# Kernel optimization log

Hardware: AMD Instinct MI355X
Metric: run time of the kernel (lower is better)

Reference implementation:

```python
import jax, jax.numpy as jnp
import numpy as np

N_P, N_A = 200_000, 100_000
D_P, D_A, H, OUT = 64, 64, 32, 1
E_PP, E_AP, E_PA = 3_200_000, 1_600_000, 1_600_000


def _lin(key, din, dout, bias=True):
    kw, kb = jax.random.split(key)
    W = jax.random.normal(kw, (din, dout), jnp.float32) * (1.0 / np.sqrt(din))
    if bias:
        b = jax.random.normal(kb, (dout,), jnp.float32) * 0.01
        return W, b
    return W


def setup_inputs() -> dict:
    key = jax.random.key(0)
    ks = jax.random.split(key, 24)
    inp = {}
    inp['x_paper'] = jax.random.normal(ks[0], (N_P, D_P), jnp.float32)
    inp['x_author'] = jax.random.normal(ks[1], (N_A, D_A), jnp.float32)
    inp['src_pp'] = jax.random.randint(ks[2], (E_PP,), 0, N_P)
    inp['dst_pp'] = jax.random.randint(ks[3], (E_PP,), 0, N_P)
    inp['src_ap'] = jax.random.randint(ks[4], (E_AP,), 0, N_A)
    inp['dst_ap'] = jax.random.randint(ks[5], (E_AP,), 0, N_P)
    inp['src_pa'] = jax.random.randint(ks[6], (E_PA,), 0, N_P)
    inp['dst_pa'] = jax.random.randint(ks[7], (E_PA,), 0, N_A)
    # Layer-1 SAGEConv weights per relation: lin_l (neighbor, with bias), lin_r (root, no bias)
    inp['Wl1_pp'], inp['bl1_pp'] = _lin(ks[8], D_P, H)
    inp['Wr1_pp'] = _lin(ks[9], D_P, H, bias=False)
    inp['Wl1_ap'], inp['bl1_ap'] = _lin(ks[10], D_A, H)
    inp['Wr1_ap'] = _lin(ks[11], D_P, H, bias=False)
    inp['Wl1_pa'], inp['bl1_pa'] = _lin(ks[12], D_P, H)
    inp['Wr1_pa'] = _lin(ks[13], D_A, H, bias=False)
    # Layer-2 SAGEConv weights (only relations feeding 'paper' affect the output)
    inp['Wl2_pp'], inp['bl2_pp'] = _lin(ks[14], H, H)
    inp['Wr2_pp'] = _lin(ks[15], H, H, bias=False)
    inp['Wl2_ap'], inp['bl2_ap'] = _lin(ks[16], H, H)
    inp['Wr2_ap'] = _lin(ks[17], H, H, bias=False)
    # Final classifier Linear(32, 1)
    inp['W_lin'], inp['b_lin'] = _lin(ks[18], H, OUT)
    return inp


def _sage_rel(x_src, x_dst, src, dst, Wl, bl, Wr):
    # SAGEConv: lin_l(mean_{j in N(i)} x_j) + lin_r(x_i)
    n_dst = x_dst.shape[0]
    agg = jax.ops.segment_sum(x_src[src], dst, num_segments=n_dst)
    cnt = jax.ops.segment_sum(jnp.ones((src.shape[0],), x_src.dtype), dst, num_segments=n_dst)
    mean = agg / jnp.maximum(cnt, 1.0)[:, None]
    return mean @ Wl + bl + x_dst @ Wr


def reference(x_paper, x_author, src_pp, dst_pp, src_ap, dst_ap, src_pa, dst_pa,
              Wl1_pp, bl1_pp, Wr1_pp, Wl1_ap, bl1_ap, Wr1_ap, Wl1_pa, bl1_pa, Wr1_pa,
              Wl2_pp, bl2_pp, Wr2_pp, Wl2_ap, bl2_ap, Wr2_ap, W_lin, b_lin):
    # Layer 1 (to_hetero: sum per-relation conv outputs per destination type), then relu
    p1 = (_sage_rel(x_paper, x_paper, src_pp, dst_pp, Wl1_pp, bl1_pp, Wr1_pp)
          + _sage_rel(x_author, x_paper, src_ap, dst_ap, Wl1_ap, bl1_ap, Wr1_ap))
    a1 = _sage_rel(x_paper, x_author, src_pa, dst_pa, Wl1_pa, bl1_pa, Wr1_pa)
    p1, a1 = jax.nn.relu(p1), jax.nn.relu(a1)
    # Layer 2: only 'paper' output is consumed downstream
    p2 = (_sage_rel(p1, p1, src_pp, dst_pp, Wl2_pp, bl2_pp, Wr2_pp)
          + _sage_rel(a1, p1, src_ap, dst_ap, Wl2_ap, bl2_ap, Wr2_ap))
    # model_config is None -> plain Linear, no sigmoid/softmax
    return p2 @ W_lin + b_lin
```

## Files before the change

kernel.cpp:

```cpp
#include <hip/hip_runtime.h>


typedef unsigned short ushort_t;
typedef __attribute__((ext_vector_type(8))) short bf16x8;
typedef __attribute__((ext_vector_type(4))) float f32x4;

#define PWBITS 9
#define PWIN   (1 << PWBITS)
#define PCHUNK 4096
#define CAPPAD 2048
#define FW_R   12

__device__ inline ushort_t f2bf(float f) {
    unsigned u = __float_as_uint(f);
    unsigned r = (u + 0x7FFFu + ((u >> 16) & 1u)) >> 16;
    return (ushort_t)r;
}
__device__ inline float bf2f_lo(unsigned u) { return __uint_as_float(u << 16); }
__device__ inline float bf2f_hi(unsigned u) { return __uint_as_float(u & 0xFFFF0000u); }
__device__ inline int ntl(const int* p) { return __builtin_nontemporal_load(p); }

__global__ void prep_weights(
    const float* __restrict__ Wl1_pp, const float* __restrict__ Wr1_pp,
    const float* __restrict__ Wl1_ap, const float* __restrict__ Wr1_ap,
    const float* __restrict__ Wl1_pa, const float* __restrict__ Wr1_pa,
    const float* __restrict__ bl1_pp, const float* __restrict__ bl1_ap,
    const float* __restrict__ bl1_pa,
    const float* __restrict__ Wl2_pp, const float* __restrict__ bl2_pp,
    const float* __restrict__ Wr2_pp,
    const float* __restrict__ Wl2_ap, const float* __restrict__ bl2_ap,
    const float* __restrict__ Wr2_ap,
    const float* __restrict__ W_lin, const float* __restrict__ b_lin,
    float* __restrict__ Wcomb_p, float* __restrict__ Wcomb_a,
    ushort_t* __restrict__ Wfrag_p, ushort_t* __restrict__ Wfrag_a,
    float* __restrict__ bias_p, float* __restrict__ bias_a,
    float* __restrict__ vv)
{
    int t = threadIdx.x;
    for (int idx = t; idx < 64 * 96; idx += 256) {
        int i = idx / 96, j = idx % 96;
        float v;
        if (j < 32)       v = Wl1_pp[i * 32 + j];
        else if (j < 64)  v = Wl1_pa[i * 32 + (j - 32)];
        else              v = Wr1_pp[i * 32 + (j - 64)] + Wr1_ap[i * 32 + (j - 64)];
        Wcomb_p[idx] = v;
    }
    for (int idx = t; idx < 64 * 64; idx += 256) {
        int i = idx / 64, j = idx % 64;
        Wcomb_a[idx] = (j < 32) ? Wl1_ap[i * 32 + j] : Wr1_pa[i * 32 + (j - 32)];
    }
    if (t < 32) {
        bias_p[t] = bl1_pp[t] + bl1_ap[t];
        bias_a[t] = bl1_pa[t];
        float vpp = 0.f, vr = 0.f, vap = 0.f;
        for (int j = 0; j < 32; ++j) {
            float wl = W_lin[j];
            vpp += Wl2_pp[t * 32 + j] * wl;
            vr  += (Wr2_pp[t * 32 + j] + Wr2_ap[t * 32 + j]) * wl;
            vap += Wl2_ap[t * 32 + j] * wl;
        }
        vv[t] = vpp; vv[32 + t] = vr; vv[96 + t] = vap;
    }
    if (t == 0) {
        float c = b_lin[0];
        for (int j = 0; j < 32; ++j) c += (bl2_pp[j] + bl2_ap[j]) * W_lin[j];
        vv[64] = c;
    }
    __syncthreads();
    for (int idx = t; idx < 12 * 64 * 8; idx += 256) {
        int f = idx >> 9, l = (idx >> 3) & 63, j = idx & 7;
        int nt = f >> 1, kh = f & 1;
        int k = kh * 32 + 8 * (l >> 4) + j;
        int n = nt * 16 + (l & 15);
        Wfrag_p[idx] = f2bf(Wcomb_p[k * 96 + n]);
    }
    for (int idx = t; idx < 8 * 64 * 8; idx += 256) {
        int f = idx >> 9, l = (idx >> 3) & 63, j = idx & 7;
        int nt = f >> 1, kh = f & 1;
        int k = kh * 32 + 8 * (l >> 4) + j;
        int n = nt * 16 + (l & 15);
        Wfrag_a[idx] = f2bf(Wcomb_a[k * 64 + n]);
    }
}

__device__ inline void partition_body(
    int b, int nb0, int nb1,
    const int* __restrict__ src0, const int* __restrict__ dst0, int E0,
    unsigned* __restrict__ bk0, int cap0, int nw0, int* __restrict__ wc0,
    const int* __restrict__ src1, const int* __restrict__ dst1, int E1,
    unsigned* __restrict__ bk1, int cap1, int nw1, int* __restrict__ wc1,
    const int* __restrict__ src2, const int* __restrict__ dst2, int E2,
    unsigned* __restrict__ bk2, int cap2, int nw2, int* __restrict__ wc2,
    int* lcnt, int* lbase)
{
    const int* src; const int* dst; int E; unsigned* bk; int cap; int nw; int* wc; int chunk;
    if (b < nb0)            { src = src0; dst = dst0; E = E0; bk = bk0; cap = cap0; nw = nw0; wc = wc0; chunk = b; }
    else if (b < nb0 + nb1) { src = src1; dst = dst1; E = E1; bk = bk1; cap = cap1; nw = nw1; wc = wc1; chunk = b - nb0; }
    else                    { src = src2; dst = dst2; E = E2; bk = bk2; cap = cap2; nw = nw2; wc = wc2; chunk = b - nb0 - nb1; }
    int e0 = chunk * PCHUNK;
    int d_[16], s_[16];
#pragma unroll
    for (int r = 0; r < 4; ++r) {
        int base = e0 + r * 1024 + threadIdx.x * 4;
        if (base + 3 < E) {
            int4 dv = *(const int4*)(dst + base);
            int4 sv = *(const int4*)(src + base);
            d_[r * 4 + 0] = dv.x; d_[r * 4 + 1] = dv.y; d_[r * 4 + 2] = dv.z; d_[r * 4 + 3] = dv.w;
            s_[r * 4 + 0] = sv.x; s_[r * 4 + 1] = sv.y; s_[r * 4 + 2] = sv.z; s_[r * 4 + 3] = sv.w;
        } else {
#pragma unroll
            for (int k = 0; k < 4; ++k) {
                int e = base + k;
                d_[r * 4 + k] = (e < E) ? dst[e] : -1;
                s_[r * 4 + k] = 0;
            }
        }
    }
    for (int i = threadIdx.x; i < nw; i += 256) lcnt[i] = 0;
    __syncthreads();
#pragma unroll
    for (int k = 0; k < 16; ++k)
        if (d_[k] >= 0) atomicAdd(&lcnt[((unsigned)d_[k]) >> PWBITS], 1);
    __syncthreads();
    for (int i = threadIdx.x; i < nw; i += 256) {
        int c = lcnt[i];
        lbase[i] = (c > 0) ? atomicAdd(&wc[i * 16], c) : 0;
        lcnt[i] = 0;
    }
    __syncthreads();
#pragma unroll
    for (int k = 0; k < 16; ++k) {
        int d = d_[k];
        if (d >= 0) {
            int w = ((unsigned)d) >> PWBITS;
            int off = lbase[w] + atomicAdd(&lcnt[w], 1);
            if (off < cap)
                bk[(size_t)w * cap + off] =
                    (((unsigned)(d & (PWIN - 1))) << 18) | (unsigned)s_[k];
        }
    }
}

__device__ inline bf16x8 cvt8(const float* p) {
    float4 a = *(const float4*)p;
    float4 b = *(const float4*)(p + 4);
    bf16x8 r;
    r[0] = (short)f2bf(a.x); r[1] = (short)f2bf(a.y);
    r[2] = (short)f2bf(a.z); r[3] = (short)f2bf(a.w);
    r[4] = (short)f2bf(b.x); r[5] = (short)f2bf(b.y);
    r[6] = (short)f2bf(b.z); r[7] = (short)f2bf(b.w);
    return r;
}

__device__ inline void proj_paper_body(
    int blk, const float* __restrict__ x, const ushort_t* __restrict__ Wfrag,
    const float* __restrict__ bias,
    ushort_t* __restrict__ h_pp, ushort_t* __restrict__ h_pa,
    float* __restrict__ root_p, int N)
{
    int wave = threadIdx.x >> 6, lane = threadIdx.x & 63;
    int mbase = blk * 64 + wave * 16;
    int row = lane & 15, grp = lane >> 4;
    int nA = mbase + row; if (nA > N - 1) nA = N - 1;
    const float* xr = x + (size_t)nA * 64 + grp * 8;
    bf16x8 a0 = cvt8(xr);
    bf16x8 a1 = cvt8(xr + 32);
    f32x4 acc0 = {0.f, 0.f, 0.f, 0.f}, acc1 = acc0, acc2 = acc0, acc3 = acc0;
    float bp0 = bias[row];
    float bp1 = bias[16 + row];
    f32x4 acc4 = {bp0, bp0, bp0, bp0};
    f32x4 acc5 = {bp1, bp1, bp1, bp1};
    const bf16x8* wf = (const bf16x8*)(Wfrag) + lane;
    acc0 = __builtin_amdgcn_mfma_f32_16x16x32_bf16(a0, wf[0 * 64], acc0, 0, 0, 0);
    acc0 = __builtin_amdgcn_mfma_f32_16x16x32_bf16(a1, wf[1 * 64], acc0, 0, 0, 0);
    acc1 = __builtin_amdgcn_mfma_f32_16x16x32_bf16(a0, wf[2 * 64], acc1, 0, 0, 0);
    acc1 = __builtin_amdgcn_mfma_f32_16x16x32_bf16(a1, wf[3 * 64], acc1, 0, 0, 0);
    acc2 = __builtin_amdgcn_mfma_f32_16x16x32_bf16(a0, wf[4 * 64], acc2, 0, 0, 0);
    acc2 = __builtin_amdgcn_mfma_f32_16x16x32_bf16(a1, wf[5 * 64], acc2, 0, 0, 0);
    acc3 = __builtin_amdgcn_mfma_f32_16x16x32_bf16(a0, wf[6 * 64], acc3, 0, 0, 0);
    acc3 = __builtin_amdgcn_mfma_f32_16x16x32_bf16(a1, wf[7 * 64], acc3, 0, 0, 0);
    acc4 = __builtin_amdgcn_mfma_f32_16x16x32_bf16(a0, wf[8 * 64], acc4, 0, 0, 0);
    acc4 = __builtin_amdgcn_mfma_f32_16x16x32_bf16(a1, wf[9 * 64], acc4, 0, 0, 0);
    acc5 = __builtin_amdgcn_mfma_f32_16x16x32_bf16(a0, wf[10 * 64], acc5, 0, 0, 0);
    acc5 = __builtin_amdgcn_mfma_f32_16x16x32_bf16(a1, wf[11 * 64], acc5, 0, 0, 0);
    int node0 = mbase + grp * 4;
#pragma unroll
    for (int reg = 0; reg < 4; ++reg) {
        int nd = node0 + reg;
        if (nd < N) {
            size_t b32 = (size_t)nd * 32;
            h_pp[b32 + row]        = f2bf(acc0[reg]);
            h_pp[b32 + 16 + row]   = f2bf(acc1[reg]);
            h_pa[b32 + row]        = f2bf(acc2[reg]);
            h_pa[b32 + 16 + row]   = f2bf(acc3[reg]);
            root_p[b32 + row]      = acc4[reg];
            root_p[b32 + 16 + row] = acc5[reg];
        }
    }
}

__device__ inline void proj_author_body(
    int blk, const float* __restrict__ x, const ushort_t* __restrict__ Wfrag,
    const float* __restrict__ bias,
    ushort_t* __restrict__ h_ap, float* __restrict__ root_a, int N)
{
    int wave = threadIdx.x >> 6, lane = threadIdx.x & 63;
    int mbase = blk * 64 + wave * 16;
    int row = lane & 15, grp = lane >> 4;
    int nA = mbase + row; if (nA > N - 1) nA = N - 1;
    const float* xr = x + (size_t)nA * 64 + grp * 8;
    bf16x8 a0 = cvt8(xr);
    bf16x8 a1 = cvt8(xr + 32);
    f32x4 acc0 = {0.f, 0.f, 0.f, 0.f}, acc1 = acc0;
    float bp0 = bias[row];
    float bp1 = bias[16 + row];
    f32x4 acc2 = {bp0, bp0, bp0, bp0};
    f32x4 acc3 = {bp1, bp1, bp1, bp1};
    const bf16x8* wf = (const bf16x8*)(Wfrag) + lane;
    acc0 = __builtin_amdgcn_mfma_f32_16x16x32_bf16(a0, wf[0 * 64], acc0, 0, 0, 0);
    acc0 = __builtin_amdgcn_mfma_f32_16x16x32_bf16(a1, wf[1 * 64], acc0, 0, 0, 0);
    acc1 = __builtin_amdgcn_mfma_f32_16x16x32_bf16(a0, wf[2 * 64], acc1, 0, 0, 0);
    acc1 = __builtin_amdgcn_mfma_f32_16x16x32_bf16(a1, wf[3 * 64], acc1, 0, 0, 0);
    acc2 = __builtin_amdgcn_mfma_f32_16x16x32_bf16(a0, wf[4 * 64], acc2, 0, 0, 0);
    acc2 = __builtin_amdgcn_mfma_f32_16x16x32_bf16(a1, wf[5 * 64], acc2, 0, 0, 0);
    acc3 = __builtin_amdgcn_mfma_f32_16x16x32_bf16(a0, wf[6 * 64], acc3, 0, 0, 0);
    acc3 = __builtin_amdgcn_mfma_f32_16x16x32_bf16(a1, wf[7 * 64], acc3, 0, 0, 0);
    int node0 = mbase + grp * 4;
#pragma unroll
    for (int reg = 0; reg < 4; ++reg) {
        int nd = node0 + reg;
        if (nd < N) {
            size_t b32 = (size_t)nd * 32;
            h_ap[b32 + row]        = f2bf(acc0[reg]);
            h_ap[b32 + 16 + row]   = f2bf(acc1[reg]);
            root_a[b32 + row]      = acc2[reg];
            root_a[b32 + 16 + row] = acc3[reg];
        }
    }
}

__global__ __launch_bounds__(256)
void part_proj(
    const int* __restrict__ src0, const int* __restrict__ dst0, int E0,
    unsigned* __restrict__ bk0, int cap0, int nw0, int* __restrict__ wc0,
    const int* __restrict__ src1, const int* __restrict__ dst1, int E1,
    unsigned* __restrict__ bk1, int cap1, int nw1, int* __restrict__ wc1,
    const int* __restrict__ src2, const int* __restrict__ dst2, int E2,
    unsigned* __restrict__ bk2, int cap2, int nw2, int* __restrict__ wc2,
    const float* __restrict__ xp, const float* __restrict__ xa,
    const ushort_t* __restrict__ Wfp, const ushort_t* __restrict__ Wfa,
    const float* __restrict__ bias_p, const float* __restrict__ bias_a,
    ushort_t* __restrict__ h_pp, ushort_t* __restrict__ h_pa,
    ushort_t* __restrict__ h_ap,
    float* __restrict__ root_p, float* __restrict__ root_a,
    int NP, int NA, int nbt, int pbp)
{
    __shared__ int lcnt[PWIN];
    __shared__ int lbase[PWIN];
    int b = blockIdx.x;
    int nb0 = (E0 + PCHUNK - 1) / PCHUNK;
    int nb1 = (E1 + PCHUNK - 1) / PCHUNK;
    if (b < nbt) {
        partition_body(b, nb0, nb1,
                       src0, dst0, E0, bk0, cap0, nw0, wc0,
                       src1, dst1, E1, bk1, cap1, nw1, wc1,
                       src2, dst2, E2, bk2, cap2, nw2, wc2, lcnt, lbase);
    } else if (b < nbt + pbp) {
        proj_paper_body(b - nbt, xp, Wfp, bias_p, h_pp, h_pa, root_p, NP);
    } else {
        proj_author_body(b - nbt - pbp, xa, Wfa, bias_a, h_ap, root_a, NA);
    }
}

__global__ __launch_bounds__(256)
void partition3(
    const int* __restrict__ src0, const int* __restrict__ dst0, int E0,
    unsigned* __restrict__ bk0, int cap0, int nw0, int* __restrict__ wc0,
    const int* __restrict__ src1, const int* __restrict__ dst1, int E1,
    unsigned* __restrict__ bk1, int cap1, int nw1, int* __restrict__ wc1,
    const int* __restrict__ src2, const int* __restrict__ dst2, int E2,
    unsigned* __restrict__ bk2, int cap2, int nw2, int* __restrict__ wc2)
{
    __shared__ int lcnt[PWIN];
    __shared__ int lbase[PWIN];
    int nb0 = (E0 + PCHUNK - 1) / PCHUNK;
    int nb1 = (E1 + PCHUNK - 1) / PCHUNK;
    partition_body(blockIdx.x, nb0, nb1,
                   src0, dst0, E0, bk0, cap0, nw0, wc0,
                   src1, dst1, E1, bk1, cap1, nw1, wc1,
                   src2, dst2, E2, bk2, cap2, nw2, wc2, lcnt, lbase);
}

__global__ __launch_bounds__(256)
void proj_all(const float* __restrict__ xp, const float* __restrict__ xa,
              const ushort_t* __restrict__ Wfp, const ushort_t* __restrict__ Wfa,
              const float* __restrict__ bias_p, const float* __restrict__ bias_a,
              ushort_t* __restrict__ h_pp, ushort_t* __restrict__ h_pa,
              ushort_t* __restrict__ h_ap,
              float* __restrict__ root_p, float* __restrict__ root_a,
              int NP, int NA, int pbp)
{
    if (blockIdx.x < pbp)
        proj_paper_body(blockIdx.x, xp, Wfp, bias_p, h_pp, h_pa, root_p, NP);
    else
        proj_author_body(blockIdx.x - pbp, xa, Wfa, bias_a, h_ap, root_a, NA);
}

__global__ __launch_bounds__(256)
void fill_win3(
    const unsigned* __restrict__ bk0, const int* __restrict__ wc0, int cap0,
    int* __restrict__ csr0, int* __restrict__ cnt0, int* __restrict__ rs0, int N0, int nw0,
    const unsigned* __restrict__ bk1, const int* __restrict__ wc1, int cap1,
    int* __restrict__ csr1, int* __restrict__ cnt1, int* __restrict__ rs1, int N1, int nw1,
    const unsigned* __restrict__ bk2, const int* __restrict__ wc2, int cap2,
    int* __restrict__ csr2, int* __restrict__ cnt2, int* __restrict__ rs2, int N2, int nw2)
{
    __shared__ int lc[PWIN];
    __shared__ int wsum[4], wpre[4];
    int b = blockIdx.x;
    const unsigned* bk; const int* wc; int cap; int* csr; int* cnt; int* rs; int N; int w;
    if (b < nw0)            { bk = bk0; wc = wc0; cap = cap0; csr = csr0; cnt = cnt0; rs = rs0; N = N0; w = b; }
    else if (b < nw0 + nw1) { bk = bk1; wc = wc1; cap = cap1; csr = csr1; cnt = cnt1; rs = rs1; N = N1; w = b - nw0; }
    else                    { bk = bk2; wc = wc2; cap = cap2; csr = csr2; cnt = cnt2; rs = rs2; N = N2; w = b - nw0 - nw1; }
    int d0 = w << PWBITS;
    int sz = wc[w * 16]; if (sz > cap) sz = cap;
    const unsigned* bkt = bk + (size_t)w * cap;
    uint4 u[FW_R];
#pragma unroll
    for (int r = 0; r < FW_R; ++r) {
        int i4 = r * 1024 + threadIdx.x * 4;
        if (i4 + 3 < sz) {
            u[r] = *(const uint4*)(bkt + i4);
        } else {
            u[r].x = (i4 + 0 < sz) ? bkt[i4 + 0] : 0xFFFFFFFFu;
            u[r].y = (i4 + 1 < sz) ? bkt[i4 + 1] : 0xFFFFFFFFu;
            u[r].z = (i4 + 2 < sz) ? bkt[i4 + 2] : 0xFFFFFFFFu;
            u[r].w = (i4 + 3 < sz) ? bkt[i4 + 3] : 0xFFFFFFFFu;
        }
    }
    for (int i = threadIdx.x; i < PWIN; i += 256) lc[i] = 0;
    __syncthreads();
#pragma unroll
    for (int r = 0; r < FW_R; ++r) {
        if (u[r].x != 0xFFFFFFFFu) atomicAdd(&lc[u[r].x >> 18], 1);
        if (u[r].y != 0xFFFFFFFFu) atomicAdd(&lc[u[r].y >> 18], 1);
        if (u[r].z != 0xFFFFFFFFu) atomicAdd(&lc[u[r].z >> 18], 1);
        if (u[r].w != 0xFFFFFFFFu) atomicAdd(&lc[u[r].w >> 18], 1);
    }
    __syncthreads();
    {
        int i = threadIdx.x * 2;
        int d = d0 + i;
        if (d < N)     cnt[d] = lc[i];
        if (d + 1 < N) cnt[d + 1] = lc[i + 1];
    }
    int t2 = threadIdx.x * 2;
    int v0 = lc[t2], v1 = lc[t2 + 1];
    int ts = v0 + v1;
    int lane = threadIdx.x & 63;
    int wid = threadIdx.x >> 6;
    int incl = ts;
#pragma unroll
    for (int off = 1; off < 64; off <<= 1) {
        int o = __shfl_up(incl, off);
        if (lane >= off) incl += o;
    }
    if (lane == 63) wsum[wid] = incl;
    __syncthreads();
    if (threadIdx.x == 0) {
        int r = 0;
        for (int i = 0; i < 4; ++i) { wpre[i] = r; r += wsum[i]; }
    }
    __syncthreads();
    int run = w * cap + wpre[wid] + (incl - ts);
    lc[t2] = run;
    if (d0 + t2 < N) rs[d0 + t2] = run;
    run += v0;
    lc[t2 + 1] = run;
    if (d0 + t2 + 1 < N) rs[d0 + t2 + 1] = run;
    __syncthreads();
#pragma unroll
    for (int r = 0; r < FW_R; ++r) {
        if (u[r].x != 0xFFFFFFFFu) { int p = atomicAdd(&lc[u[r].x >> 18], 1); csr[p] = (int)(u[r].x & 0x3FFFFu); }
        if (u[r].y != 0xFFFFFFFFu) { int p = atomicAdd(&lc[u[r].y >> 18], 1); csr[p] = (int)(u[r].y & 0x3FFFFu); }
        if (u[r].z != 0xFFFFFFFFu) { int p = atomicAdd(&lc[u[r].z >> 18], 1); csr[p] = (int)(u[r].z & 0x3FFFFu); }
        if (u[r].w != 0xFFFFFFFFu) { int p = atomicAdd(&lc[u[r].w >> 18], 1); csr[p] = (int)(u[r].w & 0x3FFFFu); }
    }
}

#define ACC8(A, U) \
    A[0] += bf2f_lo((U).x); A[1] += bf2f_hi((U).x); \
    A[2] += bf2f_lo((U).y); A[3] += bf2f_hi((U).y); \
    A[4] += bf2f_lo((U).z); A[5] += bf2f_hi((U).z); \
    A[6] += bf2f_lo((U).w); A[7] += bf2f_hi((U).w);

__global__ __launch_bounds__(256, 8)
void pull_paper(const ushort_t* __restrict__ h_pp, const ushort_t* __restrict__ h_ap,
                const float* __restrict__ root,
                const int* __restrict__ csr_pp, const int* __restrict__ rs_pp,
                const int* __restrict__ cnt_pp,
                const int* __restrict__ csr_ap, const int* __restrict__ rs_ap,
                const int* __restrict__ cnt_ap,
                const float* __restrict__ vv,
                float* __restrict__ s_pp, float* __restrict__ out, int N)
{
    __shared__ float v0[32], v1[32];
    __shared__ float c2s;
    if (threadIdx.x < 32) { v0[threadIdx.x] = vv[threadIdx.x]; v1[threadIdx.x] = vv[32 + threadIdx.x]; }
    if (threadIdx.x == 0) c2s = vv[64];
    __syncthreads();
    int n = blockIdx.x * 64 + (threadIdx.x >> 2);
    if (n >= N) return;
    int c = threadIdx.x & 3;
    float a[8];
#pragma unroll
    for (int k = 0; k < 8; ++k) a[k] = 0.f;
    int s1 = rs_pp[n], k1 = cnt_pp[n], e1 = s1 + k1;
    int j = s1;
    for (; j + 4 <= e1; j += 4) {
        int i0 = ntl(csr_pp + j), i1 = ntl(csr_pp + j + 1);
        int i2 = ntl(csr_pp + j + 2), i3 = ntl(csr_pp + j + 3);
        uint4 u0 = ((const uint4*)(h_pp + (size_t)i0 * 32))[c];
        uint4 u1 = ((const uint4*)(h_pp + (size_t)i1 * 32))[c];
        uint4 u2 = ((const uint4*)(h_pp + (size_t)i2 * 32))[c];
        uint4 u3 = ((const uint4*)(h_pp + (size_t)i3 * 32))[c];
        ACC8(a, u0) ACC8(a, u1) ACC8(a, u2) ACC8(a, u3)
    }
    for (; j < e1; ++j) {
        uint4 u0 = ((const uint4*)(h_pp + (size_t)ntl(csr_pp + j) * 32))[c];
        ACC8(a, u0)
    }
    float b[8];
#pragma unroll
    for (int k = 0; k < 8; ++k) b[k] = 0.f;
    int s2 = rs_ap[n], k2 = cnt_ap[n], e2 = s2 + k2;
    j = s2;
    for (; j + 4 <= e2; j += 4) {
        int i0 = ntl(csr_ap + j), i1 = ntl(csr_ap + j + 1);
        int i2 = ntl(csr_ap + j + 2), i3 = ntl(csr_ap + j + 3);
        uint4 u0 = ((const uint4*)(h_ap + (size_t)i0 * 32))[c];
        uint4 u1 = ((const uint4*)(h_ap + (size_t)i1 * 32))[c];
        uint4 u2 = ((const uint4*)(h_ap + (size_t)i2 * 32))[c];
        uint4 u3 = ((const uint4*)(h_ap + (size_t)i3 * 32))[c];
        ACC8(b, u0) ACC8(b, u1) ACC8(b, u2) ACC8(b, u3)
    }
    for (; j < e2; ++j) {
        uint4 u0 = ((const uint4*)(h_ap + (size_t)ntl(csr_ap + j) * 32))[c];
        ACC8(b, u0)
    }
    float ipp = 1.0f / fmaxf((float)k1, 1.0f);
    float iap = 1.0f / fmaxf((float)k2, 1.0f);
    const float* rt = root + (size_t)n * 32 + 8 * c;
    float d0 = 0.f, d1 = 0.f;
#pragma unroll
    for (int k = 0; k < 8; ++k) {
        float p = fmaxf(rt[k] + a[k] * ipp + b[k] * iap, 0.f);
        d0 += p * v0[8 * c + k];
        d1 += p * v1[8 * c + k];
    }
    d0 += __shfl_xor(d0, 1); d0 += __shfl_xor(d0, 2);
    d1 += __shfl_xor(d1, 1); d1 += __shfl_xor(d1, 2);
    if (c == 0) { s_pp[n] = d0; out[n] = d1 + c2s; }
}

__global__ __launch_bounds__(256, 8)
void pull_author(const ushort_t* __restrict__ h_pa, const float* __restrict__ root,
                 const int* __restrict__ csr_pa, const int* __restrict__ rs_pa,
                 const int* __restrict__ cnt_pa,
                 const float* __restrict__ vv, float* __restrict__ s_ap, int N)
{
    __shared__ float v0[32];
    if (threadIdx.x < 32) v0[threadIdx.x] = vv[96 + threadIdx.x];
    __syncthreads();
    int n = blockIdx.x * 64 + (threadIdx.x >> 2);
    if (n >= N) return;
    int c = threadIdx.x & 3;
    float a[8];
#pragma unroll
    for (int k = 0; k < 8; ++k) a[k] = 0.f;
    int s1 = rs_pa[n], k1 = cnt_pa[n], e1 = s1 + k1;
    int j = s1;
    for (; j + 4 <= e1; j += 4) {
        int i0 = ntl(csr_pa + j), i1 = ntl(csr_pa + j + 1);
        int i2 = ntl(csr_pa + j + 2), i3 = ntl(csr_pa + j + 3);
        uint4 u0 = ((const uint4*)(h_pa + (size_t)i0 * 32))[c];
        uint4 u1 = ((const uint4*)(h_pa + (size_t)i1 * 32))[c];
        uint4 u2 = ((const uint4*)(h_pa + (size_t)i2 * 32))[c];
        uint4 u3 = ((const uint4*)(h_pa + (size_t)i3 * 32))[c];
        ACC8(a, u0) ACC8(a, u1) ACC8(a, u2) ACC8(a, u3)
    }
    for (; j < e1; ++j) {
        uint4 u0 = ((const uint4*)(h_pa + (size_t)ntl(csr_pa + j) * 32))[c];
        ACC8(a, u0)
    }
    float ip = 1.0f / fmaxf((float)k1, 1.0f);
    const float* rt = root + (size_t)n * 32 + 8 * c;
    float d0 = 0.f;
#pragma unroll
    for (int k = 0; k < 8; ++k) {
        float p = fmaxf(rt[k] + a[k] * ip, 0.f);
        d0 += p * v0[8 * c + k];
    }
    d0 += __shfl_xor(d0, 1); d0 += __shfl_xor(d0, 2);
    if (c == 0) s_ap[n] = d0;
}

__global__ __launch_bounds__(256, 8)
void pull2(const float* __restrict__ s_pp, const float* __restrict__ s_ap,
           const int* __restrict__ csr_pp, const int* __restrict__ rs_pp,
           const int* __restrict__ cnt_pp,
           const int* __restrict__ csr_ap, const int* __restrict__ rs_ap,
           const int* __restrict__ cnt_ap,
           float* __restrict__ out, int N)
{
    int g = (blockIdx.x * blockDim.x + threadIdx.x) >> 2;
    int c = threadIdx.x & 3;
    if (g >= N) return;
    int s1 = rs_pp[g], k1 = cnt_pp[g], e1 = s1 + k1;
    float t = 0.f;
    for (int j = s1 + c; j < e1; j += 4) t += s_pp[ntl(csr_pp + j)];
    int s2 = rs_ap[g], k2 = cnt_ap[g], e2 = s2 + k2;
    float u = 0.f;
    for (int j = s2 + c; j < e2; j += 4) u += s_ap[ntl(csr_ap + j)];
    t += __shfl_xor(t, 1); t += __shfl_xor(t, 2);
    u += __shfl_xor(u, 1); u += __shfl_xor(u, 2);
    if (c == 0) {
        out[g] += t / fmaxf((float)k1, 1.f) + u / fmaxf((float)k2, 1.f);
    }
}

extern "C" void kernel_launch(void* const* d_in, const int* in_sizes, int n_in,
                              void* d_out, int out_size, void* d_ws, size_t ws_size,
                              hipStream_t stream)
{
    const float* x_paper  = (const float*)d_in[0];
    const float* x_author = (const float*)d_in[1];
    const int* src_pp = (const int*)d_in[2];
    const int* dst_pp = (const int*)d_in[3];
    const int* src_ap = (const int*)d_in[4];
    const int* dst_ap = (const int*)d_in[5];
    const int* src_pa = (const int*)d_in[6];
    const int* dst_pa = (const int*)d_in[7];
    const float* Wl1_pp = (const float*)d_in[8];
    const float* bl1_pp = (const float*)d_in[9];
    const float* Wr1_pp = (const float*)d_in[10];
    const float* Wl1_ap = (const float*)d_in[11];
    const float* bl1_ap = (const float*)d_in[12];
    const float* Wr1_ap = (const float*)d_in[13];
    const float* Wl1_pa = (const float*)d_in[14];
    const float* bl1_pa = (const float*)d_in[15];
    const float* Wr1_pa = (const float*)d_in[16];
    const float* Wl2_pp = (const float*)d_in[17];
    const float* bl2_pp = (const float*)d_in[18];
    const float* Wr2_pp = (const float*)d_in[19];
    const float* Wl2_ap = (const float*)d_in[20];
    const float* bl2_ap = (const float*)d_in[21];
    const float* Wr2_ap = (const float*)d_in[22];
    const float* W_lin  = (const float*)d_in[23];
    const float* b_lin  = (const float*)d_in[24];

    const int NP = in_sizes[0] / 64;
    const int NA = in_sizes[1] / 64;
    const int E_PP = in_sizes[2];
    const int E_AP = in_sizes[4];
    const int E_PA = in_sizes[6];

    const int nw_pp = (NP + PWIN - 1) >> PWBITS;
    const int nw_ap = nw_pp;
    const int nw_pa = (NA + PWIN - 1) >> PWBITS;
    const int cap_pp = ((E_PP / nw_pp + CAPPAD) + 3) & ~3;
    const int cap_ap = ((E_AP / nw_ap + CAPPAD) + 3) & ~3;
    const int cap_pa = ((E_PA / nw_pa + CAPPAD) + 3) & ~3;

    char* wp = (char*)d_ws;
    int* wcur = (int*)wp;             wp += (size_t)3 * PWIN * 16 * 4;
    unsigned* bk_pp = (unsigned*)wp;  wp += (size_t)nw_pp * cap_pp * 4;
    unsigned* bk_ap = (unsigned*)wp;  wp += (size_t)nw_ap * cap_ap * 4;
    unsigned* bk_pa = (unsigned*)wp;  wp += (size_t)nw_pa * cap_pa * 4;
    int* csr_pp = (int*)wp;           wp += (size_t)nw_pp * cap_pp * 4;
    int* csr_ap = (int*)wp;           wp += (size_t)nw_ap * cap_ap * 4;
    int* csr_pa = (int*)wp;           wp += (size_t)nw_pa * cap_pa * 4;
    int* cnt    = (int*)wp;           wp += (size_t)(2 * NP + NA) * 4;
    int* rs     = (int*)wp;           wp += (size_t)(2 * NP + NA) * 4;
    ushort_t* h_pp = (ushort_t*)wp;   wp += (size_t)NP * 32 * 2;
    ushort_t* h_pa = (ushort_t*)wp;   wp += (size_t)NP * 32 * 2;
    ushort_t* h_ap = (ushort_t*)wp;   wp += (size_t)NA * 32 * 2;
    float* root_a = (float*)wp;       wp += (size_t)NA * 32 * 4;
    float* s_pp   = (float*)wp;       wp += (size_t)NP * 4;
    float* s_ap   = (float*)wp;       wp += (size_t)NA * 4;
    float* Wcomb_p = (float*)wp;      wp += 64 * 96 * 4;
    float* Wcomb_a = (float*)wp;      wp += 64 * 64 * 4;
    ushort_t* Wfrag_p = (ushort_t*)wp; wp += 12 * 64 * 8 * 2;
    ushort_t* Wfrag_a = (ushort_t*)wp; wp += 8 * 64 * 8 * 2;
    float* bias_p = (float*)wp;       wp += 32 * 4;
    float* bias_a = (float*)wp;       wp += 32 * 4;
    float* vv     = (float*)wp;       wp += 128 * 4;
    size_t used = (size_t)(wp - (char*)d_ws);
    size_t rootp_bytes = (size_t)NP * 32 * 4;
    bool fused = (used + rootp_bytes) <= ws_size;
    float* root_p = fused ? (float*)wp : (float*)bk_pp;

    int* cnt_pp = cnt,  * cnt_ap = cnt + NP,  * cnt_pa = cnt + 2 * NP;
    int* rs_pp  = rs,   * rs_ap  = rs + NP,   * rs_pa  = rs + 2 * NP;

    float* out = (float*)d_out;

    hipMemsetAsync(wcur, 0, (size_t)3 * PWIN * 16 * 4, stream);

    prep_weights<<<1, 256, 0, stream>>>(
        Wl1_pp, Wr1_pp, Wl1_ap, Wr1_ap, Wl1_pa, Wr1_pa,
        bl1_pp, bl1_ap, bl1_pa,
        Wl2_pp, bl2_pp, Wr2_pp, Wl2_ap, bl2_ap, Wr2_ap,
        W_lin, b_lin, Wcomb_p, Wcomb_a, Wfrag_p, Wfrag_a, bias_p, bias_a, vv);

    int nb_total = (E_PP + PCHUNK - 1) / PCHUNK + (E_AP + PCHUNK - 1) / PCHUNK
                 + (E_PA + PCHUNK - 1) / PCHUNK;
    int pbp = (NP + 63) / 64;
    int pba = (NA + 63) / 64;

    if (fused) {
        part_proj<<<nb_total + pbp + pba, 256, 0, stream>>>(
            src_pp, dst_pp, E_PP, bk_pp, cap_pp, nw_pp, wcur + 0,
            src_ap, dst_ap, E_AP, bk_ap, cap_ap, nw_ap, wcur + PWIN * 16,
            src_pa, dst_pa, E_PA, bk_pa, cap_pa, nw_pa, wcur + 2 * PWIN * 16,
            x_paper, x_author, Wfrag_p, Wfrag_a, bias_p, bias_a,
            h_pp, h_pa, h_ap, root_p, root_a, NP, NA, nb_total, pbp);

        fill_win3<<<nw_pp + nw_ap + nw_pa, 256, 0, stream>>>(
            bk_pp, wcur + 0,             cap_pp, csr_pp, cnt_pp, rs_pp, NP, nw_pp,
            bk_ap, wcur + PWIN * 16,     cap_ap, csr_ap, cnt_ap, rs_ap, NP, nw_ap,
            bk_pa, wcur + 2 * PWIN * 16, cap_pa, csr_pa, cnt_pa, rs_pa, NA, nw_pa);
    } else {
        partition3<<<nb_total, 256, 0, stream>>>(
            src_pp, dst_pp, E_PP, bk_pp, cap_pp, nw_pp, wcur + 0,
            src_ap, dst_ap, E_AP, bk_ap, cap_ap, nw_ap, wcur + PWIN * 16,
            src_pa, dst_pa, E_PA, bk_pa, cap_pa, nw_pa, wcur + 2 * PWIN * 16);

        fill_win3<<<nw_pp + nw_ap + nw_pa, 256, 0, stream>>>(
            bk_pp, wcur + 0,             cap_pp, csr_pp, cnt_pp, rs_pp, NP, nw_pp,
            bk_ap, wcur + PWIN * 16,     cap_ap, csr_ap, cnt_ap, rs_ap, NP, nw_ap,
            bk_pa, wcur + 2 * PWIN * 16, cap_pa, csr_pa, cnt_pa, rs_pa, NA, nw_pa);

        proj_all<<<pbp + pba, 256, 0, stream>>>(
            x_paper, x_author, Wfrag_p, Wfrag_a, bias_p, bias_a,
            h_pp, h_pa, h_ap, root_p, root_a, NP, NA, pbp);
    }

    pull_paper<<<(NP + 63) / 64, 256, 0, stream>>>(
        h_pp, h_ap, root_p, csr_pp, rs_pp, cnt_pp, csr_ap, rs_ap, cnt_ap,
        vv, s_pp, out, NP);
    pull_author<<<(NA + 63) / 64, 256, 0, stream>>>(
        h_pa, root_a, csr_pa, rs_pa, cnt_pa, vv, s_ap, NA);

    pull2<<<((size_t)NP * 4 + 255) / 256, 256, 0, stream>>>(
        s_pp, s_ap, csr_pp, rs_pp, cnt_pp, csr_ap, rs_ap, cnt_ap, out, NP);
}
```

Before: 367.6 us.

## Fuse projection blocks with CSR fill instead of with edge partition

Before, the node projection GEMM blocks ran in the same launch as the edge partition pass, and the CSR window fill ran in a separate launch afterward. Now partition runs alone, and the projection blocks share a launch with the window-fill blocks. This pairs the atomic-heavy, LDS-bound fill blocks with MFMA/bandwidth projection blocks, and leaves partition with full occupancy. The fallback path reuses the fused kernel with block counts chosen so only one role runs per launch. The risk is that fill is shorter or less parallel than partition (a few hundred blocks), which would hide less of the projection work than before.

```diff
diff --git a/kernel.cpp b/kernel.cpp
--- a/kernel.cpp
+++ b/kernel.cpp
@@ -83,16 +83,20 @@
     }
 }
 
-__device__ inline void partition_body(
-    int b, int nb0, int nb1,
+__global__ __launch_bounds__(256)
+void partition3(
     const int* __restrict__ src0, const int* __restrict__ dst0, int E0,
     unsigned* __restrict__ bk0, int cap0, int nw0, int* __restrict__ wc0,
     const int* __restrict__ src1, const int* __restrict__ dst1, int E1,
     unsigned* __restrict__ bk1, int cap1, int nw1, int* __restrict__ wc1,
     const int* __restrict__ src2, const int* __restrict__ dst2, int E2,
-    unsigned* __restrict__ bk2, int cap2, int nw2, int* __restrict__ wc2,
-    int* lcnt, int* lbase)
-{
+    unsigned* __restrict__ bk2, int cap2, int nw2, int* __restrict__ wc2)
+{
+    __shared__ int lcnt[PWIN];
+    __shared__ int lbase[PWIN];
+    int nb0 = (E0 + PCHUNK - 1) / PCHUNK;
+    int nb1 = (E1 + PCHUNK - 1) / PCHUNK;
+    int b = blockIdx.x;
     const int* src; const int* dst; int E; unsigned* bk; int cap; int nw; int* wc; int chunk;
     if (b < nb0)            { src = src0; dst = dst0; E = E0; bk = bk0; cap = cap0; nw = nw0; wc = wc0; chunk = b; }
     else if (b < nb0 + nb1) { src = src1; dst = dst1; E = E1; bk = bk1; cap = cap1; nw = nw1; wc = wc1; chunk = b - nb0; }
@@ -138,6 +142,77 @@
                 bk[(size_t)w * cap + off] =
                     (((unsigned)(d & (PWIN - 1))) << 18) | (unsigned)s_[k];
         }
+    }
+}
+
+__device__ inline void fill_body(
+    int b, const unsigned* __restrict__ bk, const int* __restrict__ wc, int cap,
+    int* __restrict__ csr, int* __restrict__ cnt, int* __restrict__ rs,
+    int N, int w, int* lc, int* wsum, int* wpre)
+{
+    int d0 = w << PWBITS;
+    int sz = wc[w * 16]; if (sz > cap) sz = cap;
+    const unsigned* bkt = bk + (size_t)w * cap;
+    uint4 u[FW_R];
+#pragma unroll
+    for (int r = 0; r < FW_R; ++r) {
+        int i4 = r * 1024 + threadIdx.x * 4;
+        if (i4 + 3 < sz) {
+            u[r] = *(const uint4*)(bkt + i4);
+        } else {
+            u[r].x = (i4 + 0 < sz) ? bkt[i4 + 0] : 0xFFFFFFFFu;
+            u[r].y = (i4 + 1 < sz) ? bkt[i4 + 1] : 0xFFFFFFFFu;
+            u[r].z = (i4 + 2 < sz) ? bkt[i4 + 2] : 0xFFFFFFFFu;
+            u[r].w = (i4 + 3 < sz) ? bkt[i4 + 3] : 0xFFFFFFFFu;
+        }
+    }
+    for (int i = threadIdx.x; i < PWIN; i += 256) lc[i] = 0;
+    __syncthreads();
+#pragma unroll
+    for (int r = 0; r < FW_R; ++r) {
+        if (u[r].x != 0xFFFFFFFFu) atomicAdd(&lc[u[r].x >> 18], 1);
+        if (u[r].y != 0xFFFFFFFFu) atomicAdd(&lc[u[r].y >> 18], 1);
+        if (u[r].z != 0xFFFFFFFFu) atomicAdd(&lc[u[r].z >> 18], 1);
+        if (u[r].w != 0xFFFFFFFFu) atomicAdd(&lc[u[r].w >> 18], 1);
+    }
+    __syncthreads();
+    {
+        int i = threadIdx.x * 2;
+        int d = d0 + i;
+        if (d < N)     cnt[d] = lc[i];
+        if (d + 1 < N) cnt[d + 1] = lc[i + 1];
+    }
+    int t2 = threadIdx.x * 2;
+    int v0 = lc[t2], v1 = lc[t2 + 1];
+    int ts = v0 + v1;
+    int lane = threadIdx.x & 63;
+    int wid = threadIdx.x >> 6;
+    int incl = ts;
+#pragma unroll
+    for (int off = 1; off < 64; off <<= 1) {
+        int o = __shfl_up(incl, off);
+        if (lane >= off) incl += o;
+    }
+    if (lane == 63) wsum[wid] = incl;
+    __syncthreads();
+    if (threadIdx.x == 0) {
+        int r = 0;
+        for (int i = 0; i < 4; ++i) { wpre[i] = r; r += wsum[i]; }
+    }
+    __syncthreads();
+    int run = w * cap + wpre[wid] + (incl - ts);
+    lc[t2] = run;
+    if (d0 + t2 < N) rs[d0 + t2] = run;
+    run += v0;
+    lc[t2 + 1] = run;
+    if (d0 + t2 + 1 < N) rs[d0 + t2 + 1] = run;
+    __syncthreads();
+#pragma unroll
+    for (int r = 0; r < FW_R; ++r) {
+        if (u[r].x != 0xFFFFFFFFu) { int p = atomicAdd(&lc[u[r].x >> 18], 1); csr[p] = (int)(u[r].x & 0x3FFFFu); }
+        if (u[r].y != 0xFFFFFFFFu) { int p = atomicAdd(&lc[u[r].y >> 18], 1); csr[p] = (int)(u[r].y & 0x3FFFFu); }
+        if (u[r].z != 0xFFFFFFFFu) { int p = atomicAdd(&lc[u[r].z >> 18], 1); csr[p] = (int)(u[r].z & 0x3FFFFu); }
+        if (u[r].w != 0xFFFFFFFFu) { int p = atomicAdd(&lc[u[r].w >> 18], 1); csr[p] = (int)(u[r].w & 0x3FFFFu); }
     }
 }
 
@@ -240,151 +315,35 @@
 }
 
 __global__ __launch_bounds__(256)
-void part_proj(
-    const int* __restrict__ src0, const int* __restrict__ dst0, int E0,
-    unsigned* __restrict__ bk0, int cap0, int nw0, int* __restrict__ wc0,
-    const int* __restrict__ src1, const int* __restrict__ dst1, int E1,
-    unsigned* __restrict__ bk1, int cap1, int nw1, int* __restrict__ wc1,
-    const int* __restrict__ src2, const int* __restrict__ dst2, int E2,
-    unsigned* __restrict__ bk2, int cap2, int nw2, int* __restrict__ wc2,
+void fill_proj(
+    const unsigned* __restrict__ bk0, const int* __restrict__ wc0, int cap0,
+    int* __restrict__ csr0, int* __restrict__ cnt0, int* __restrict__ rs0, int N0, int nw0,
+    const unsigned* __restrict__ bk1, const int* __restrict__ wc1, int cap1,
+    int* __restrict__ csr1, int* __restrict__ cnt1, int* __restrict__ rs1, int N1, int nw1,
+    const unsigned* __restrict__ bk2, const int* __restrict__ wc2, int cap2,
+    int* __restrict__ csr2, int* __restrict__ cnt2, int* __restrict__ rs2, int N2, int nw2,
     const float* __restrict__ xp, const float* __restrict__ xa,
     const ushort_t* __restrict__ Wfp, const ushort_t* __restrict__ Wfa,
     const float* __restrict__ bias_p, const float* __restrict__ bias_a,
     ushort_t* __restrict__ h_pp, ushort_t* __restrict__ h_pa,
     ushort_t* __restrict__ h_ap,
     float* __restrict__ root_p, float* __restrict__ root_a,
-    int NP, int NA, int nbt, int pbp)
-{
-    __shared__ int lcnt[PWIN];
-    __shared__ int lbase[PWIN];
-    int b = blockIdx.x;
-    int nb0 = (E0 + PCHUNK - 1) / PCHUNK;
-    int nb1 = (E1 + PCHUNK - 1) / PCHUNK;
-    if (b < nbt) {
-        partition_body(b, nb0, nb1,
-                       src0, dst0, E0, bk0, cap0, nw0, wc0,
-                       src1, dst1, E1, bk1, cap1, nw1, wc1,
-                       src2, dst2, E2, bk2, cap2, nw2, wc2, lcnt, lbase);
-    } else if (b < nbt + pbp) {
-        proj_paper_body(b - nbt, xp, Wfp, bias_p, h_pp, h_pa, root_p, NP);
-    } else {
-        proj_author_body(b - nbt - pbp, xa, Wfa, bias_a, h_ap, root_a, NA);
-    }
-}
-
-__global__ __launch_bounds__(256)
-void partition3(
-    const int* __restrict__ src0, const int* __restrict__ dst0, int E0,
-    unsigned* __restrict__ bk0, int cap0, int nw0, int* __restrict__ wc0,
-    const int* __restrict__ src1, const int* __restrict__ dst1, int E1,
-    unsigned* __restrict__ bk1, int cap1, int nw1, int* __restrict__ wc1,
-    const int* __restrict__ src2, const int* __restrict__ dst2, int E2,
-    unsigned* __restrict__ bk2, int cap2, int nw2, int* __restrict__ wc2)
-{
-    __shared__ int lcnt[PWIN];
-    __shared__ int lbase[PWIN];
-    int nb0 = (E0 + PCHUNK - 1) / PCHUNK;
-    int nb1 = (E1 + PCHUNK - 1) / PCHUNK;
-    partition_body(blockIdx.x, nb0, nb1,
-                   src0, dst0, E0, bk0, cap0, nw0, wc0,
-                   src1, dst1, E1, bk1, cap1, nw1, wc1,
-                   src2, dst2, E2, bk2, cap2, nw2, wc2, lcnt, lbase);
-}
-
-__global__ __launch_bounds__(256)
-void proj_all(const float* __restrict__ xp, const float* __restrict__ xa,
-              const ushort_t* __restrict__ Wfp, const ushort_t* __restrict__ Wfa,
-              const float* __restrict__ bias_p, const float* __restrict__ bias_a,
-              ushort_t* __restrict__ h_pp, ushort_t* __restrict__ h_pa,
-              ushort_t* __restrict__ h_ap,
-              float* __restrict__ root_p, float* __restrict__ root_a,
-              int NP, int NA, int pbp)
-{
-    if (blockIdx.x < pbp)
-        proj_paper_body(blockIdx.x, xp, Wfp, bias_p, h_pp, h_pa, root_p, NP);
-    else
-        proj_author_body(blockIdx.x - pbp, xa, Wfa, bias_a, h_ap, root_a, NA);
-}
-
-__global__ __launch_bounds__(256)
-void fill_win3(
-    const unsigned* __restrict__ bk0, const int* __restrict__ wc0, int cap0,
-    int* __restrict__ csr0, int* __restrict__ cnt0, int* __restrict__ rs0, int N0, int nw0,
-    const unsigned* __restrict__ bk1, const int* __restrict__ wc1, int cap1,
-    int* __restrict__ csr1, int* __restrict__ cnt1, int* __restrict__ rs1, int N1, int nw1,
-    const unsigned* __restrict__ bk2, const int* __restrict__ wc2, int cap2,
-    int* __restrict__ csr2, int* __restrict__ cnt2, int* __restrict__ rs2, int N2, int nw2)
+    int NP, int NA, int pbp)
 {
     __shared__ int lc[PWIN];
     __shared__ int wsum[4], wpre[4];
     int b = blockIdx.x;
-    const unsigned* bk; const int* wc; int cap; int* csr; int* cnt; int* rs; int N; int w;
-    if (b < nw0)            { bk = bk0; wc = wc0; cap = cap0; csr = csr0; cnt = cnt0; rs = rs0; N = N0; w = b; }
-    else if (b < nw0 + nw1) { bk = bk1; wc = wc1; cap = cap1; csr = csr1; cnt = cnt1; rs = rs1; N = N1; w = b - nw0; }
-    else                    { bk = bk2; wc = wc2; cap = cap2; csr = csr2; cnt = cnt2; rs = rs2; N = N2; w = b - nw0 - nw1; }
-    int d0 = w << PWBITS;
-    int sz = wc[w * 16]; if (sz > cap) sz = cap;
-    const unsigned* bkt = bk + (size_t)w * cap;
-    uint4 u[FW_R];
-#pragma unroll
-    for (int r = 0; r < FW_R; ++r) {
-        int i4 = r * 1024 + threadIdx.x * 4;
-        if (i4 + 3 < sz) {
-            u[r] = *(const uint4*)(bkt + i4);
-        } else {
-            u[r].x = (i4 + 0 < sz) ? bkt[i4 + 0] : 0xFFFFFFFFu;
-            u[r].y = (i4 + 1 < sz) ? bkt[i4 + 1] : 0xFFFFFFFFu;
-            u[r].z = (i4 + 2 < sz) ? bkt[i4 + 2] : 0xFFFFFFFFu;
-            u[r].w = (i4 + 3 < sz) ? bkt[i4 + 3] : 0xFFFFFFFFu;
-        }
-    }
-    for (int i = threadIdx.x; i < PWIN; i += 256) lc[i] = 0;
-    __syncthreads();
-#pragma unroll
-    for (int r = 0; r < FW_R; ++r) {
-        if (u[r].x != 0xFFFFFFFFu) atomicAdd(&lc[u[r].x >> 18], 1);
-        if (u[r].y != 0xFFFFFFFFu) atomicAdd(&lc[u[r].y >> 18], 1);
-        if (u[r].z != 0xFFFFFFFFu) atomicAdd(&lc[u[r].z >> 18], 1);
-        if (u[r].w != 0xFFFFFFFFu) atomicAdd(&lc[u[r].w >> 18], 1);
-    }
-    __syncthreads();
-    {
-        int i = threadIdx.x * 2;
-        int d = d0 + i;
-        if (d < N)     cnt[d] = lc[i];
-        if (d + 1 < N) cnt[d + 1] = lc[i + 1];
-    }
-    int t2 = threadIdx.x * 2;
-    int v0 = lc[t2], v1 = lc[t2 + 1];
-    int ts = v0 + v1;
-    int lane = threadIdx.x & 63;
-    int wid = threadIdx.x >> 6;
-    int incl = ts;
-#pragma unroll
-    for (int off = 1; off < 64; off <<= 1) {
-        int o = __shfl_up(incl, off);
-        if (lane >= off) incl += o;
-    }
-    if (lane == 63) wsum[wid] = incl;
-    __syncthreads();
-    if (threadIdx.x == 0) {
-        int r = 0;
-        for (int i = 0; i < 4; ++i) { wpre[i] = r; r += wsum[i]; }
-    }
-    __syncthreads();
-    int run = w * cap + wpre[wid] + (incl - ts);
-    lc[t2] = run;
-    if (d0 + t2 < N) rs[d0 + t2] = run;
-    run += v0;
-    lc[t2 + 1] = run;
-    if (d0 + t2 + 1 < N) rs[d0 + t2 + 1] = run;
-    __syncthreads();
-#pragma unroll
-    for (int r = 0; r < FW_R; ++r) {
-        if (u[r].x != 0xFFFFFFFFu) { int p = atomicAdd(&lc[u[r].x >> 18], 1); csr[p] = (int)(u[r].x & 0x3FFFFu); }
-        if (u[r].y != 0xFFFFFFFFu) { int p = atomicAdd(&lc[u[r].y >> 18], 1); csr[p] = (int)(u[r].y & 0x3FFFFu); }
-        if (u[r].z != 0xFFFFFFFFu) { int p = atomicAdd(&lc[u[r].z >> 18], 1); csr[p] = (int)(u[r].z & 0x3FFFFu); }
-        if (u[r].w != 0xFFFFFFFFu) { int p = atomicAdd(&lc[u[r].w >> 18], 1); csr[p] = (int)(u[r].w & 0x3FFFFu); }
+    int nwt = nw0 + nw1 + nw2;
+    if (b < nwt) {
+        const unsigned* bk; const int* wc; int cap; int* csr; int* cnt; int* rs; int N; int w;
+        if (b < nw0)            { bk = bk0; wc = wc0; cap = cap0; csr = csr0; cnt = cnt0; rs = rs0; N = N0; w = b; }
+        else if (b < nw0 + nw1) { bk = bk1; wc = wc1; cap = cap1; csr = csr1; cnt = cnt1; rs = rs1; N = N1; w = b - nw0; }
+        else                    { bk = bk2; wc = wc2; cap = cap2; csr = csr2; cnt = cnt2; rs = rs2; N = N2; w = b - nw0 - nw1; }
+        fill_body(b, bk, wc, cap, csr, cnt, rs, N, w, lc, wsum, wpre);
+    } else if (b < nwt + pbp) {
+        proj_paper_body(b - nwt, xp, Wfp, bias_p, h_pp, h_pa, root_p, NP);
+    } else {
+        proj_author_body(b - nwt - pbp, xa, Wfa, bias_a, h_ap, root_a, NA);
     }
 }
 
@@ -597,8 +556,8 @@
     float* vv     = (float*)wp;       wp += 128 * 4;
     size_t used = (size_t)(wp - (char*)d_ws);
     size_t rootp_bytes = (size_t)NP * 32 * 4;
-    bool fused = (used + rootp_bytes) <= ws_size;
-    float* root_p = fused ? (float*)wp : (float*)bk_pp;
+    bool roomy = (used + rootp_bytes) <= ws_size;
+    float* root_p = roomy ? (float*)wp : (float*)bk_pp;
 
     int* cnt_pp = cnt,  * cnt_ap = cnt + NP,  * cnt_pa = cnt + 2 * NP;
     int* rs_pp  = rs,   * rs_ap  = rs + NP,   * rs_pa  = rs + 2 * NP;
@@ -617,31 +576,31 @@
                  + (E_PA + PCHUNK - 1) / PCHUNK;
     int pbp = (NP + 63) / 64;
     int pba = (NA + 63) / 64;
-
-    if (fused) {
-        part_proj<<<nb_total + pbp + pba, 256, 0, stream>>>(
-            src_pp, dst_pp, E_PP, bk_pp, cap_pp, nw_pp, wcur + 0,
-            src_ap, dst_ap, E_AP, bk_ap, cap_ap, nw_ap, wcur + PWIN * 16,
-            src_pa, dst_pa, E_PA, bk_pa, cap_pa, nw_pa, wcur + 2 * PWIN * 16,
-            x_paper, x_author, Wfrag_p, Wfrag_a, bias_p, bias_a,
-            h_pp, h_pa, h_ap, root_p, root_a, NP, NA, nb_total, pbp);
-
-        fill_win3<<<nw_pp + nw_ap + nw_pa, 256, 0, stream>>>(
+    int nwt = nw_pp + nw_ap + nw_pa;
+
+    partition3<<<nb_total, 256, 0, stream>>>(
+        src_pp, dst_pp, E_PP, bk_pp, cap_pp, nw_pp, wcur + 0,
+        src_ap, dst_ap, E_AP, bk_ap, cap_ap, nw_ap, wcur + PWIN * 16,
+        src_pa, dst_pa, E_PA, bk_pa, cap_pa, nw_pa, wcur + 2 * PWIN * 16);
+
+    if (roomy) {
+        fill_proj<<<nwt + pbp + pba, 256, 0, stream>>>(
             bk_pp, wcur + 0,             cap_pp, csr_pp, cnt_pp, rs_pp, NP, nw_pp,
             bk_ap, wcur + PWIN * 16,     cap_ap, csr_ap, cnt_ap, rs_ap, NP, nw_ap,
-            bk_pa, wcur + 2 * PWIN * 16, cap_pa, csr_pa, cnt_pa, rs_pa, NA, nw_pa);
+            bk_pa, wcur + 2 * PWIN * 16, cap_pa, csr_pa, cnt_pa, rs_pa, NA, nw_pa,
+            x_paper, x_author, Wfrag_p, Wfrag_a, bias_p, bias_a,
+            h_pp, h_pa, h_ap, root_p, root_a, NP, NA, pbp);
     } else {
-        partition3<<<nb_total, 256, 0, stream>>>(
-            src_pp, dst_pp, E_PP, bk_pp, cap_pp, nw_pp, wcur + 0,
-            src_ap, dst_ap, E_AP, bk_ap, cap_ap, nw_ap, wcur + PWIN * 16,
-            src_pa, dst_pa, E_PA, bk_pa, cap_pa, nw_pa, wcur + 2 * PWIN * 16);
-
-        fill_win3<<<nw_pp + nw_ap + nw_pa, 256, 0, stream>>>(
+        fill_proj<<<nwt, 256, 0, stream>>>(
             bk_pp, wcur + 0,             cap_pp, csr_pp, cnt_pp, rs_pp, NP, nw_pp,
             bk_ap, wcur + PWIN * 16,     cap_ap, csr_ap, cnt_ap, rs_ap, NP, nw_ap,
-            bk_pa, wcur + 2 * PWIN * 16, cap_pa, csr_pa, cnt_pa, rs_pa, NA, nw_pa);
-
-        proj_all<<<pbp + pba, 256, 0, stream>>>(
+            bk_pa, wcur + 2 * PWIN * 16, cap_pa, csr_pa, cnt_pa, rs_pa, NA, nw_pa,
+            x_paper, x_author, Wfrag_p, Wfrag_a, bias_p, bias_a,
+            h_pp, h_pa, h_ap, root_p, root_a, NP, NA, 0x40000000);
+        fill_proj<<<pbp + pba, 256, 0, stream>>>(
+            bk_pp, wcur + 0,             cap_pp, csr_pp, cnt_pp, rs_pp, NP, 0,
+            bk_ap, wcur + PWIN * 16,     cap_ap, csr_ap, cnt_ap, rs_ap, NP, 0,
+            bk_pa, wcur + 2 * PWIN * 16, cap_pa, csr_pa, cnt_pa, rs_pa, NA, 0,
             x_paper, x_author, Wfrag_p, Wfrag_a, bias_p, bias_a,
             h_pp, h_pa, h_ap, root_p, root_a, NP, NA, pbp);
     }
```

Measured after the change: 373.7 us. Within noise of the previous version (+1.7%).
